# Kernel tuning notes

Hardware: AMD Instinct MI355X
Metric: run time of the kernel (lower is better)

## Reference

```python
import jax, jax.numpy as jnp
import numpy as np

B, T, D, H = 2, 2048, 1024, 16
HD = D // H  # 64


def setup_inputs() -> dict:
    key = jax.random.key(0)
    ks = jax.random.split(key, 9)
    w = lambda k, shp: (jax.random.normal(k, shp, jnp.float32) * 0.02)
    return {
        "x": jax.random.normal(ks[0], (B, T, D), jnp.float32),
        "Wq": w(ks[1], (D, D)), "bq": jnp.zeros((D,), jnp.float32),
        "Wk": w(ks[2], (D, D)), "bk": jnp.zeros((D,), jnp.float32),
        "Wv": w(ks[3], (D, D)), "bv": jnp.zeros((D,), jnp.float32),
        "Wo": w(ks[4], (D, D)), "bo": jnp.zeros((D,), jnp.float32),
        "Wqs": w(ks[5], (3, HD)), "bqs": jnp.zeros((3,), jnp.float32),
        "Wks": w(ks[6], (3, HD)), "bks": jnp.zeros((3,), jnp.float32),
        "Wvs": w(ks[7], (3, HD)), "bvs": jnp.zeros((3,), jnp.float32),
        "temp": jnp.float32(1.0),
    }


def reference(x, Wq, bq, Wk, bk, Wv, bv, Wo, bo, Wqs, bqs, Wks, bks, Wvs, bvs, temp):
    Bx, Tx, Dx = x.shape
    # project and split heads: [B,H,T,HD]
    split = lambda y: y.reshape(Bx, Tx, H, HD).transpose(0, 2, 1, 3)
    q = split(x @ Wq.T + bq)
    k = split(x @ Wk.T + bk)
    v = split(x @ Wv.T + bv)
    # STP projections to 3-d: [B,H,T,3]
    q_stp = q @ Wqs.T + bqs
    k3 = k @ Wks.T + bks
    v3 = v @ Wvs.T + bvs
    # cross-product term (note: original's layernormed k_sub/v_sub are dead code)
    cross_kv = jnp.cross(k3, v3, axis=-1)  # [B,H,T,3]
    scores = (jnp.einsum('bhqd,bhkd->bhqk', q, k)
              + jnp.einsum('bhqc,bhkc->bhqk', q_stp, cross_kv)) * temp
    attn = jax.nn.softmax(scores, axis=-1)
    out = jnp.einsum('bhqk,bhkd->bhqd', attn, v)  # [B,H,T,HD]
    out = out.transpose(0, 2, 1, 3).reshape(Bx, Tx, Dx)
    return out @ Wo.T + bo
```

## Files before the change

### kernel.cpp

```cpp
#include <hip/hip_runtime.h>
#include <stdint.h>

typedef unsigned short u16;
typedef unsigned int u32;
typedef __attribute__((ext_vector_type(8))) short bf16x8;
typedef __attribute__((ext_vector_type(4))) float f32x4;
typedef __attribute__((ext_vector_type(4))) unsigned int u32x4;

__device__ __forceinline__ u16 f2b(float f) {
    union { float f; u32 u; } t; t.f = f;
    return (u16)((t.u + 0x7FFFu + ((t.u >> 16) & 1u)) >> 16);
}
__device__ __forceinline__ u32 pack2(float a, float b) {
    return (u32)f2b(a) | ((u32)f2b(b) << 16);
}
__device__ __forceinline__ u32 cvtpk2(float lo, float hi) {
    u32 r;
    asm("v_cvt_pk_bf16_f32 %0, %1, %2" : "=v"(r) : "v"(lo), "v"(hi));
    return r;
}
__device__ __forceinline__ void permlane32_swap(u32& a, u32& b) {
    asm("v_permlane32_swap_b32 %0, %1" : "+v"(a), "+v"(b));
}
__device__ __forceinline__ void permlane16_swap(u32& a, u32& b) {
    asm("v_permlane16_swap_b32 %0, %1" : "+v"(a), "+v"(b));
}

__device__ __forceinline__ void async_cp16(const u16* g, const u16* lds_base) {
    __builtin_amdgcn_global_load_lds(
        (const __attribute__((address_space(1))) void*)(uintptr_t)g,
        (__attribute__((address_space(3))) void*)(u32)(uintptr_t)lds_base,
        16, 0, 0);
}

__global__ void cast_all_kernel(const float* __restrict__ x,
                                const float* __restrict__ Wq, const float* __restrict__ Wk,
                                const float* __restrict__ Wv, const float* __restrict__ Wo,
                                u16* __restrict__ xb, u16* __restrict__ Wqb, u16* __restrict__ Wkb,
                                u16* __restrict__ Wvb, u16* __restrict__ Wob) {
    int i = blockIdx.x * blockDim.x + threadIdx.x;
    const float* s; u16* d; int off;
    if (i < 1048576) { s = x; d = xb; off = i; }
    else {
        int j = i - 1048576;
        int w = j >> 18; off = j & 262143;
        if (w == 0) { s = Wq; d = Wqb; }
        else if (w == 1) { s = Wk; d = Wkb; }
        else if (w == 2) { s = Wv; d = Wvb; }
        else { s = Wo; d = Wob; }
    }
    float4 f = ((const float4*)s)[off];
    ((uint2*)d)[off] = make_uint2(pack2(f.x, f.y), pack2(f.z, f.w));
}

__global__ __launch_bounds__(256) void gemm_qkv_kernel(
    const u16* __restrict__ xb,
    const u16* __restrict__ Wq, const u16* __restrict__ Wk, const u16* __restrict__ Wv,
    const float* __restrict__ bq, const float* __restrict__ bk, const float* __restrict__ bv,
    const float* __restrict__ Wqs, const float* __restrict__ bqs,
    const float* __restrict__ Wks, const float* __restrict__ bks,
    const float* __restrict__ Wvs, const float* __restrict__ bvs,
    const float* __restrict__ temp_p,
    u16* __restrict__ qe, u16* __restrict__ ke, u16* __restrict__ vT,
    float4* __restrict__ k3b, float4* __restrict__ v3b)
{
    __shared__ __align__(16) u16 As[2 * 64 * 64];
    __shared__ __align__(16) u16 Bs[2 * 128 * 64];
    const int tid = threadIdx.x;
    const int lane = tid & 63, w = tid >> 6;
    const int wm = w >> 1, wn = w & 1;
    const int l15 = lane & 15, quad = lane >> 4;
    const int lin = blockIdx.x;
    const int M0 = (lin & 63) * 64;
    const int N0 = ((lin >> 6) & 7) * 128;
    const int bz = lin >> 9;

    const u16* W = (bz == 0) ? Wq : (bz == 1) ? Wk : Wv;
    const float* bias = (bz == 0) ? bq : (bz == 1) ? bk : bv;
    const float* Wst = (bz == 0) ? Wqs : (bz == 1) ? Wks : Wvs;
    const float* bst = (bz == 0) ? bqs : (bz == 1) ? bks : bvs;

    f32x4 acc[2][4];
#pragma unroll
    for (int i = 0; i < 2; i++)
#pragma unroll
        for (int j = 0; j < 4; j++) acc[i][j] = (f32x4){0.f, 0.f, 0.f, 0.f};

    const int lr3 = lane >> 3, lp = lane & 7;
    u32 aoff[2];
#pragma unroll
    for (int j = 0; j < 2; j++) {
        int r = w * 16 + j * 8 + lr3;
        aoff[j] = (u32)(r * 1024 + ((lp ^ (r & 7)) * 8));
    }
    u32 boff[4];
#pragma unroll
    for (int j = 0; j < 4; j++) {
        int r = w * 32 + j * 8 + lr3;
        boff[j] = (u32)(r * 1024 + ((lp ^ (r & 7)) * 8));
    }
    const u16* Ag = xb + (size_t)M0 * 1024;
    const u16* Bg = W + (size_t)N0 * 1024;

#pragma unroll
    for (int j = 0; j < 2; j++) async_cp16(Ag + aoff[j], As + w * 1024 + j * 512);
#pragma unroll
    for (int j = 0; j < 4; j++) async_cp16(Bg + boff[j], Bs + w * 2048 + j * 512);
    __syncthreads();

    for (int k0 = 0; k0 < 1024; k0 += 64) {
        const int buf = (k0 >> 6) & 1;
        const u16* Asr = As + buf * 4096;
        const u16* Bsr = Bs + buf * 8192;
        if (k0 + 64 < 1024) {
            const int nb_ = buf ^ 1;
#pragma unroll
            for (int j = 0; j < 2; j++) async_cp16(Ag + (k0 + 64) + aoff[j], As + nb_ * 4096 + w * 1024 + j * 512);
#pragma unroll
            for (int j = 0; j < 4; j++) async_cp16(Bg + (k0 + 64) + boff[j], Bs + nb_ * 8192 + w * 2048 + j * 512);
        }

#pragma unroll
        for (int kk = 0; kk < 2; kk++) {
            bf16x8 af[2], bf[4];
#pragma unroll
            for (int mi = 0; mi < 2; mi++) {
                int ra = wm * 32 + mi * 16 + l15;
                af[mi] = *(const bf16x8*)(Asr + ra * 64 + (((kk * 4 + quad) ^ (ra & 7)) * 8));
            }
#pragma unroll
            for (int ni = 0; ni < 4; ni++) {
                int rb = wn * 64 + ni * 16 + l15;
                bf[ni] = *(const bf16x8*)(Bsr + rb * 64 + (((kk * 4 + quad) ^ (rb & 7)) * 8));
            }
#pragma unroll
            for (int mi = 0; mi < 2; mi++)
#pragma unroll
                for (int ni = 0; ni < 4; ni++)
                    acc[mi][ni] = __builtin_amdgcn_mfma_f32_16x16x32_bf16(af[mi], bf[ni], acc[mi][ni], 0, 0, 0);
        }

        __syncthreads();
    }

    const float tau = temp_p[0] * 1.44269504088896f;
    const int nb = N0 + wn * 64;
    const int h = nb >> 6;
    float bias_v[4], wst_v[3][4];
#pragma unroll
    for (int ni = 0; ni < 4; ni++) {
        bias_v[ni] = bias[nb + ni * 16 + l15];
#pragma unroll
        for (int c = 0; c < 3; c++) wst_v[c][ni] = Wst[c * 64 + ni * 16 + l15];
    }
    const float bst0 = bst[0], bst1 = bst[1], bst2 = bst[2];

#pragma unroll
    for (int mi = 0; mi < 2; mi++) {
        int m0 = M0 + wm * 32 + mi * 16 + quad * 4;
        int b = m0 >> 11, t0 = m0 & 2047;
        float p0[4], p1[4], p2[4];
#pragma unroll
        for (int r = 0; r < 4; r++) {
            float a0 = 0.f, a1 = 0.f, a2 = 0.f;
#pragma unroll
            for (int ni = 0; ni < 4; ni++) {
                float v = acc[mi][ni][r] + bias_v[ni];
                a0 += v * wst_v[0][ni];
                a1 += v * wst_v[1][ni];
                a2 += v * wst_v[2][ni];
            }
#pragma unroll
            for (int off = 1; off < 16; off <<= 1) {
                a0 += __shfl_xor(a0, off);
                a1 += __shfl_xor(a1, off);
                a2 += __shfl_xor(a2, off);
            }
            p0[r] = a0 + bst0; p1[r] = a1 + bst1; p2[r] = a2 + bst2;
        }

        if (bz == 0) {
#pragma unroll
            for (int r = 0; r < 4; r++) {
                size_t row = (size_t)((b * 16 + h) * 2048 + (t0 + r));
                u16* qer = qe + row * 96;
#pragma unroll
                for (int ni = 0; ni < 4; ni++)
                    qer[ni * 16 + l15] = f2b((acc[mi][ni][r] + bias_v[ni]) * tau);
                if (l15 == 0) {
                    *(u32*)(qer + 64) = pack2(p0[r] * tau, p1[r] * tau);
                    *(u32*)(qer + 66) = (u32)f2b(p2[r] * tau);
                    uint2 z = make_uint2(0u, 0u);
#pragma unroll
                    for (int j = 68; j < 96; j += 4) *(uint2*)(qer + j) = z;
                }
            }
        } else if (bz == 1) {
#pragma unroll
            for (int r = 0; r < 4; r++) {
                size_t row = (size_t)((b * 16 + h) * 2048 + (t0 + r));
                u16* ker = ke + row * 96;
#pragma unroll
                for (int ni = 0; ni < 4; ni++)
                    ker[ni * 16 + l15] = f2b(acc[mi][ni][r] + bias_v[ni]);
                if (l15 == 0)
                    k3b[row] = make_float4(p0[r], p1[r], p2[r], 0.f);
            }
        } else {
#pragma unroll
            for (int ni = 0; ni < 4; ni++) {
                int hd = ni * 16 + l15;
                float v0 = acc[mi][ni][0] + bias_v[ni];
                float v1 = acc[mi][ni][1] + bias_v[ni];
                float v2 = acc[mi][ni][2] + bias_v[ni];
                float v3 = acc[mi][ni][3] + bias_v[ni];
                *(uint2*)(vT + ((size_t)((b * 16 + h) * 64 + hd)) * 2048 + t0) =
                    make_uint2(pack2(v0, v1), pack2(v2, v3));
            }
            if (l15 == 0) {
#pragma unroll
                for (int r = 0; r < 4; r++) {
                    size_t row = (size_t)((b * 16 + h) * 2048 + (t0 + r));
                    v3b[row] = make_float4(p0[r], p1[r], p2[r], 0.f);
                }
            }
        }
    }
}

__global__ void finish_ext_kernel(const float4* __restrict__ k3b, const float4* __restrict__ v3b,
                                  u16* __restrict__ ke)
{
    int row = blockIdx.x * blockDim.x + threadIdx.x;
    if (row >= 2 * 16 * 2048) return;
    float4 k3 = k3b[row];
    float4 v3 = v3b[row];
    float c0 = k3.y * v3.z - k3.z * v3.y;
    float c1 = k3.z * v3.x - k3.x * v3.z;
    float c2 = k3.x * v3.y - k3.y * v3.x;
    u16* ker = ke + (size_t)row * 96;
    *(u32*)(ker + 64) = pack2(c0, c1);
    *(u32*)(ker + 66) = (u32)f2b(c2);
    uint2 z = make_uint2(0u, 0u);
#pragma unroll
    for (int j = 68; j < 96; j += 4) *(uint2*)(ker + j) = z;
}

__global__ __launch_bounds__(256) void gemm_out_kernel(
    const u16* __restrict__ ao, const u16* __restrict__ Wo, const float* __restrict__ bo,
    float* __restrict__ out)
{
    __shared__ __align__(16) u16 As[2 * 64 * 64];
    __shared__ __align__(16) u16 Bs[2 * 128 * 64];
    const int tid = threadIdx.x;
    const int lane = tid & 63, w = tid >> 6;
    const int wm = w >> 1, wn = w & 1;
    const int l15 = lane & 15, quad = lane >> 4;
    const int lin = blockIdx.x;
    const int M0 = (lin & 63) * 64;
    const int N0 = (lin >> 6) * 128;

    f32x4 acc[2][4];
#pragma unroll
    for (int i = 0; i < 2; i++)
#pragma unroll
        for (int j = 0; j < 4; j++) acc[i][j] = (f32x4){0.f, 0.f, 0.f, 0.f};

    const int lr3 = lane >> 3, lp = lane & 7;
    u32 aoff[2];
#pragma unroll
    for (int j = 0; j < 2; j++) {
        int r = w * 16 + j * 8 + lr3;
        aoff[j] = (u32)(r * 1024 + ((lp ^ (r & 7)) * 8));
    }
    u32 boff[4];
#pragma unroll
    for (int j = 0; j < 4; j++) {
        int r = w * 32 + j * 8 + lr3;
        boff[j] = (u32)(r * 1024 + ((lp ^ (r & 7)) * 8));
    }
    const u16* Ag = ao + (size_t)M0 * 1024;
    const u16* Bg = Wo + (size_t)N0 * 1024;

#pragma unroll
    for (int j = 0; j < 2; j++) async_cp16(Ag + aoff[j], As + w * 1024 + j * 512);
#pragma unroll
    for (int j = 0; j < 4; j++) async_cp16(Bg + boff[j], Bs + w * 2048 + j * 512);
    __syncthreads();

    for (int k0 = 0; k0 < 1024; k0 += 64) {
        const int buf = (k0 >> 6) & 1;
        const u16* Asr = As + buf * 4096;
        const u16* Bsr = Bs + buf * 8192;
        if (k0 + 64 < 1024) {
            const int nb_ = buf ^ 1;
#pragma unroll
            for (int j = 0; j < 2; j++) async_cp16(Ag + (k0 + 64) + aoff[j], As + nb_ * 4096 + w * 1024 + j * 512);
#pragma unroll
            for (int j = 0; j < 4; j++) async_cp16(Bg + (k0 + 64) + boff[j], Bs + nb_ * 8192 + w * 2048 + j * 512);
        }

#pragma unroll
        for (int kk = 0; kk < 2; kk++) {
            bf16x8 af[2], bf[4];
#pragma unroll
            for (int mi = 0; mi < 2; mi++) {
                int ra = wm * 32 + mi * 16 + l15;
                af[mi] = *(const bf16x8*)(Asr + ra * 64 + (((kk * 4 + quad) ^ (ra & 7)) * 8));
            }
#pragma unroll
            for (int ni = 0; ni < 4; ni++) {
                int rb = wn * 64 + ni * 16 + l15;
                bf[ni] = *(const bf16x8*)(Bsr + rb * 64 + (((kk * 4 + quad) ^ (rb & 7)) * 8));
            }
#pragma unroll
            for (int mi = 0; mi < 2; mi++)
#pragma unroll
                for (int ni = 0; ni < 4; ni++)
                    acc[mi][ni] = __builtin_amdgcn_mfma_f32_16x16x32_bf16(af[mi], bf[ni], acc[mi][ni], 0, 0, 0);
        }

        __syncthreads();
    }

#pragma unroll
    for (int mi = 0; mi < 2; mi++)
#pragma unroll
        for (int ni = 0; ni < 4; ni++) {
            int n = N0 + wn * 64 + ni * 16 + l15;
            float bias_n = bo[n];
            int m0 = M0 + wm * 32 + mi * 16 + quad * 4;
#pragma unroll
            for (int r = 0; r < 4; r++)
                out[(size_t)(m0 + r) * 1024 + n] = acc[mi][ni][r] + bias_n;
        }
}

__global__ __launch_bounds__(512, 2) void attn_kernel(
    const u16* __restrict__ qe, const u16* __restrict__ ke, const u16* __restrict__ vT,
    u16* __restrict__ out)
{
    __shared__ __align__(16) u16 smem[24576];
    u16* const KsA = smem;
    u16* const VtA = smem + 16384;

    const int tid = threadIdx.x;
    const int lane = tid & 63, w = tid >> 6;
    const int kw = w & 1, qw = w >> 1;
    const int l15 = lane & 15, quad = lane >> 4;
    const int lsw = l15 & 7;
    const int lin = blockIdx.x;
    const int bh = (lin & 7) + ((lin >> 3) & 3) * 8;
    const int q0 = (lin >> 5) * 128;

    const u16* qeb = qe + (size_t)bh * 2048 * 96;
    const u16* keb = ke + (size_t)bh * 2048 * 96;
    const u16* vTb = vT + (size_t)bh * 64 * 2048;

    u32 koff[2];
#pragma unroll
    for (int j = 0; j < 2; j++) {
        int r = w * 8 + j * 4 + (lane >> 4);
        int c = (lane & 15) ^ (r & 7);
        if (c >= 12) c -= 8;
        koff[j] = (u32)(r * 96 + c * 8);
    }
    u32 voff;
    {
        int r = w * 8 + (lane >> 3);
        voff = (u32)(r * 2048 + (((lane & 7) ^ (r & 7)) * 8));
    }

#pragma unroll
    for (int j = 0; j < 2; j++) async_cp16(keb + koff[j], KsA + w * 1024 + j * 512);
    async_cp16(vTb + voff, VtA + w * 512);

    bf16x8 bq[2][3];
#pragma unroll
    for (int s = 0; s < 2; s++) {
        const u16* qrow = qeb + (size_t)(q0 + qw * 32 + s * 16 + l15) * 96;
#pragma unroll
        for (int ks = 0; ks < 3; ks++) bq[s][ks] = *(const bf16x8*)(qrow + ks * 32 + quad * 8);
    }

    f32x4 O[2][4];
    float l_part[2];
#pragma unroll
    for (int s = 0; s < 2; s++) {
        l_part[s] = 0.f;
#pragma unroll
        for (int dt = 0; dt < 4; dt++) O[s][dt] = (f32x4){0.f, 0.f, 0.f, 0.f};
    }

    __syncthreads();

    for (int kb = 0; kb < 2048; kb += 64) {
        const int buf = (kb >> 6) & 1;
        const u16* Ks = KsA + buf * 8192;
        const u16* Vt = VtA + buf * 4096;

        if (kb + 64 < 2048) {
            u16* Ksn = KsA + (buf ^ 1) * 8192;
            u16* Vtn = VtA + (buf ^ 1) * 4096;
            const size_t kb96 = (size_t)(kb + 64) * 96;
#pragma unroll
            for (int j = 0; j < 2; j++) async_cp16(keb + kb96 + koff[j], Ksn + w * 1024 + j * 512);
            async_cp16(vTb + (size_t)(kb + 64) + voff, Vtn + w * 512);
        }

        f32x4 S[2][2];
#pragma unroll
        for (int s = 0; s < 2; s++)
#pragma unroll
            for (int nt = 0; nt < 2; nt++) S[s][nt] = (f32x4){0.f, 0.f, 0.f, 0.f};

        __builtin_amdgcn_s_setprio(1);
#pragma unroll
        for (int ks = 0; ks < 3; ks++) {
            bf16x8 ak[2];
#pragma unroll
            for (int nt = 0; nt < 2; nt++)
                ak[nt] = *(const bf16x8*)(Ks + (kw * 32 + nt * 16 + l15) * 128 + (((ks * 4 + quad) ^ lsw) & 15) * 8);
#pragma unroll
            for (int s = 0; s < 2; s++)
#pragma unroll
                for (int nt = 0; nt < 2; nt++)
                    S[s][nt] = __builtin_amdgcn_mfma_f32_16x16x32_bf16(ak[nt], bq[s][ks], S[s][nt], 0, 0, 0);
        }
        __builtin_amdgcn_s_setprio(0);

        bf16x8 av[4];
#pragma unroll
        for (int dt = 0; dt < 4; dt++)
            av[dt] = *(const bf16x8*)(Vt + (dt * 16 + l15) * 64 + (((kw * 4 + quad) ^ lsw) & 7) * 8);

#pragma unroll
        for (int s = 0; s < 2; s++) {
            float sum = 0.f;
#pragma unroll
            for (int nt = 0; nt < 2; nt++)
#pragma unroll
                for (int r = 0; r < 4; r++) {
                    float p = __builtin_amdgcn_exp2f(S[s][nt][r]);
                    S[s][nt][r] = p;
                    sum += p;
                }
            l_part[s] += sum;
            u32 a0 = cvtpk2(S[s][0][0], S[s][0][1]);
            u32 b0 = cvtpk2(S[s][1][0], S[s][1][1]);
            u32 a1 = cvtpk2(S[s][0][2], S[s][0][3]);
            u32 b1 = cvtpk2(S[s][1][2], S[s][1][3]);
            permlane32_swap(a0, b0);
            permlane32_swap(a1, b1);
            permlane16_swap(a0, b0);
            permlane16_swap(a1, b1);
            bf16x8 pv = __builtin_bit_cast(bf16x8, (u32x4){a0, a1, b0, b1});
            __builtin_amdgcn_s_setprio(1);
#pragma unroll
            for (int dt = 0; dt < 4; dt++)
                O[s][dt] = __builtin_amdgcn_mfma_f32_16x16x32_bf16(av[dt], pv, O[s][dt], 0, 0, 0);
            __builtin_amdgcn_s_setprio(0);
        }

        __syncthreads();
    }

    float* const Ored = (float*)smem;
    float* const Lr = (float*)(smem + 17664);
    if (kw == 1) {
#pragma unroll
        for (int s = 0; s < 2; s++) {
            float l = l_part[s];
            l += __shfl_xor(l, 16);
            l += __shfl_xor(l, 32);
            int qrow = qw * 32 + s * 16 + l15;
            if (lane < 16) Lr[qrow] = l;
#pragma unroll
            for (int dt = 0; dt < 4; dt++) {
                int dc = dt ^ (l15 & 3);
                *(float4*)(Ored + qrow * 68 + dc * 16 + quad * 4) =
                    make_float4(O[s][dt][0], O[s][dt][1], O[s][dt][2], O[s][dt][3]);
            }
        }
    }
    __syncthreads();
    if (kw == 0) {
        const int b = bh >> 4, h = bh & 15;
#pragma unroll
        for (int s = 0; s < 2; s++) {
            float l = l_part[s];
            l += __shfl_xor(l, 16);
            l += __shfl_xor(l, 32);
            int qrow = qw * 32 + s * 16 + l15;
            l += Lr[qrow];
            float linv = 1.0f / l;
            int tq = q0 + qrow;
#pragma unroll
            for (int dt = 0; dt < 4; dt++) {
                int dc = dt ^ (l15 & 3);
                float4 o2 = *(const float4*)(Ored + qrow * 68 + dc * 16 + quad * 4);
                int d = h * 64 + dt * 16 + quad * 4;
                *(uint2*)(out + (size_t)(b * 2048 + tq) * 1024 + d) =
                    make_uint2(cvtpk2((O[s][dt][0] + o2.x) * linv, (O[s][dt][1] + o2.y) * linv),
                               cvtpk2((O[s][dt][2] + o2.z) * linv, (O[s][dt][3] + o2.w) * linv));
            }
        }
    }
}

extern "C" void kernel_launch(void* const* d_in, const int* in_sizes, int n_in,
                              void* d_out, int out_size, void* d_ws, size_t ws_size,
                              hipStream_t stream)
{
    (void)in_sizes; (void)n_in; (void)out_size; (void)ws_size;
    const float* x   = (const float*)d_in[0];
    const float* Wq  = (const float*)d_in[1];
    const float* bq  = (const float*)d_in[2];
    const float* Wk  = (const float*)d_in[3];
    const float* bk  = (const float*)d_in[4];
    const float* Wv  = (const float*)d_in[5];
    const float* bv  = (const float*)d_in[6];
    const float* Wo  = (const float*)d_in[7];
    const float* bo  = (const float*)d_in[8];
    const float* Wqs = (const float*)d_in[9];
    const float* bqs = (const float*)d_in[10];
    const float* Wks = (const float*)d_in[11];
    const float* bks = (const float*)d_in[12];
    const float* Wvs = (const float*)d_in[13];
    const float* bvs = (const float*)d_in[14];
    const float* temp = (const float*)d_in[15];

    char* ws = (char*)d_ws;
    u16* xb  = (u16*)(ws);
    u16* Wqb = (u16*)(ws + 8388608);
    u16* Wkb = (u16*)(ws + 10485760);
    u16* Wvb = (u16*)(ws + 12582912);
    u16* Wob = (u16*)(ws + 14680064);
    u16* qeb = (u16*)(ws + 16777216);
    u16* keb = (u16*)(ws + 29360128);
    u16* vTb = (u16*)(ws + 41943040);
    float4* k3b = (float4*)(ws + 50331648);
    float4* v3b = (float4*)(ws + 51380224);
    u16* aob = (u16*)(ws + 52428800);

    cast_all_kernel<<<8192, 256, 0, stream>>>(x, Wq, Wk, Wv, Wo, xb, Wqb, Wkb, Wvb, Wob);
    gemm_qkv_kernel<<<1536, 256, 0, stream>>>(
        xb, Wqb, Wkb, Wvb, bq, bk, bv, Wqs, bqs, Wks, bks, Wvs, bvs, temp,
        qeb, keb, vTb, k3b, v3b);
    finish_ext_kernel<<<256, 256, 0, stream>>>(k3b, v3b, keb);
    attn_kernel<<<512, 512, 0, stream>>>(qeb, keb, vTb, aob);
    gemm_out_kernel<<<512, 256, 0, stream>>>(aob, Wob, bo, (float*)d_out);
}
```

Measured before the change: 205.8 us.

## Triple-buffer QKV GEMM with BK=32 and single barrier per step

Restructures the QKV projection GEMM main loop from a double-buffered BK=64 pipeline to a three-slot ring of BK=32 tiles. Each step uses explicit vmcnt waits and one raw s_barrier instead of two __syncthreads. A new XOR swizzle for 32-wide rows is meant to keep LDS reads conflict-free. The aim is to keep more async loads in flight and cut barrier overhead, at the cost of twice as many loop iterations, fewer MFMAs per barrier, and some risk of hazards around slot reuse.

```diff
diff --git a/kernel.cpp b/kernel.cpp
--- a/kernel.cpp
+++ b/kernel.cpp
@@ -64,8 +64,8 @@
     u16* __restrict__ qe, u16* __restrict__ ke, u16* __restrict__ vT,
     float4* __restrict__ k3b, float4* __restrict__ v3b)
 {
-    __shared__ __align__(16) u16 As[2 * 64 * 64];
-    __shared__ __align__(16) u16 Bs[2 * 128 * 64];
+    __shared__ __align__(16) u16 As[3 * 64 * 32];
+    __shared__ __align__(16) u16 Bs[3 * 128 * 32];
     const int tid = threadIdx.x;
     const int lane = tid & 63, w = tid >> 6;
     const int wm = w >> 1, wn = w & 1;
@@ -86,61 +86,45 @@
 #pragma unroll
         for (int j = 0; j < 4; j++) acc[i][j] = (f32x4){0.f, 0.f, 0.f, 0.f};
 
-    const int lr3 = lane >> 3, lp = lane & 7;
-    u32 aoff[2];
-#pragma unroll
-    for (int j = 0; j < 2; j++) {
-        int r = w * 16 + j * 8 + lr3;
-        aoff[j] = (u32)(r * 1024 + ((lp ^ (r & 7)) * 8));
-    }
-    u32 boff[4];
-#pragma unroll
-    for (int j = 0; j < 4; j++) {
-        int r = w * 32 + j * 8 + lr3;
-        boff[j] = (u32)(r * 1024 + ((lp ^ (r & 7)) * 8));
-    }
-    const u16* Ag = xb + (size_t)M0 * 1024;
-    const u16* Bg = W + (size_t)N0 * 1024;
-
-#pragma unroll
-    for (int j = 0; j < 2; j++) async_cp16(Ag + aoff[j], As + w * 1024 + j * 512);
-#pragma unroll
-    for (int j = 0; j < 4; j++) async_cp16(Bg + boff[j], Bs + w * 2048 + j * 512);
-    __syncthreads();
-
-    for (int k0 = 0; k0 < 1024; k0 += 64) {
-        const int buf = (k0 >> 6) & 1;
-        const u16* Asr = As + buf * 4096;
-        const u16* Bsr = Bs + buf * 8192;
-        if (k0 + 64 < 1024) {
-            const int nb_ = buf ^ 1;
-#pragma unroll
-            for (int j = 0; j < 2; j++) async_cp16(Ag + (k0 + 64) + aoff[j], As + nb_ * 4096 + w * 1024 + j * 512);
-#pragma unroll
-            for (int j = 0; j < 4; j++) async_cp16(Bg + (k0 + 64) + boff[j], Bs + nb_ * 8192 + w * 2048 + j * 512);
-        }
-
-#pragma unroll
-        for (int kk = 0; kk < 2; kk++) {
-            bf16x8 af[2], bf[4];
-#pragma unroll
-            for (int mi = 0; mi < 2; mi++) {
-                int ra = wm * 32 + mi * 16 + l15;
-                af[mi] = *(const bf16x8*)(Asr + ra * 64 + (((kk * 4 + quad) ^ (ra & 7)) * 8));
-            }
-#pragma unroll
-            for (int ni = 0; ni < 4; ni++) {
-                int rb = wn * 64 + ni * 16 + l15;
-                bf[ni] = *(const bf16x8*)(Bsr + rb * 64 + (((kk * 4 + quad) ^ (rb & 7)) * 8));
-            }
-#pragma unroll
-            for (int mi = 0; mi < 2; mi++)
-#pragma unroll
-                for (int ni = 0; ni < 4; ni++)
-                    acc[mi][ni] = __builtin_amdgcn_mfma_f32_16x16x32_bf16(af[mi], bf[ni], acc[mi][ni], 0, 0, 0);
-        }
-
-        __syncthreads();
+    int ra = tid >> 2, ca = ((tid & 3) ^ (ra & 3)) * 8;
+    const u16* Aga = xb + (size_t)(M0 + ra) * 1024 + ca;
+    const u16* Bg0 = W + (size_t)(N0 + ra) * 1024 + ca;
+    const u16* Bg1 = W + (size_t)(N0 + ra + 64) * 1024 + ca;
+    const int aoff = (w * 64) * 8;
+    const int boff0 = (w * 64) * 8;
+    const int boff1 = (256 + w * 64) * 8;
+
+    async_cp16(Aga, As + aoff);
+    async_cp16(Bg0, Bs + boff0);
+    async_cp16(Bg1, Bs + boff1);
+
+    for (int k0 = 0; k0 < 1024; k0 += 32) {
+        const int slot = (k0 >> 5) % 3;
+        const u16* Asr = As + slot * 2048;
+        const u16* Bsr = Bs + slot * 4096;
+        if (k0 + 32 < 1024) {
+            const int nxt = (slot == 2) ? 0 : slot + 1;
+            async_cp16(Aga + k0 + 32, As + nxt * 2048 + aoff);
+            async_cp16(Bg0 + k0 + 32, Bs + nxt * 4096 + boff0);
+            async_cp16(Bg1 + k0 + 32, Bs + nxt * 4096 + boff1);
+            asm volatile("s_waitcnt vmcnt(3)" ::: "memory");
+        } else {
+            asm volatile("s_waitcnt vmcnt(0)" ::: "memory");
+        }
+        __builtin_amdgcn_s_barrier();
+
+        bf16x8 af[2], bf[4];
+#pragma unroll
+        for (int mi = 0; mi < 2; mi++)
+            af[mi] = *(const bf16x8*)(Asr + (wm * 32 + mi * 16 + l15) * 32 + ((quad ^ (l15 & 3)) * 8));
+#pragma unroll
+        for (int ni = 0; ni < 4; ni++)
+            bf[ni] = *(const bf16x8*)(Bsr + (wn * 64 + ni * 16 + l15) * 32 + ((quad ^ (l15 & 3)) * 8));
+#pragma unroll
+        for (int mi = 0; mi < 2; mi++)
+#pragma unroll
+            for (int ni = 0; ni < 4; ni++)
+                acc[mi][ni] = __builtin_amdgcn_mfma_f32_16x16x32_bf16(af[mi], bf[ni], acc[mi][ni], 0, 0, 0);
     }
 
     const float tau = temp_p[0] * 1.44269504088896f;
```

New measurement: 217.5 us. 5.7% more time.
